# Kernel tuning notes

Hardware: AMD Instinct MI355X
Metric: run time of the kernel (lower is better)

## Reference

```python
import jax, jax.numpy as jnp
import numpy as np

N = 50000
E = 800000
D_IN = 1000
D_H2 = 128  # h_dim * multiple
D_H = 16


def gat_conv(x, src, dst, W, attn_l, attn_r, bias, n):
    """DGL-style GATConv (no dropout, no activation). Returns [n, H, F]."""
    H, F = attn_l.shape
    feat = (x @ W).reshape(n, H, F)                      # [N,H,F]
    el = jnp.sum(feat * attn_l[None], axis=-1)           # [N,H]
    er = jnp.sum(feat * attn_r[None], axis=-1)           # [N,H]
    e = jax.nn.leaky_relu(el[src] + er[dst], 0.2)        # [E,H]
    emax = jax.ops.segment_max(e, dst, num_segments=n)   # [N,H] per-dst softmax max
    ee = jnp.exp(e - emax[dst])                          # [E,H]
    denom = jax.ops.segment_sum(ee, dst, num_segments=n) # [N,H]
    alpha = ee / denom[dst]                              # [E,H]
    msg = feat[src] * alpha[..., None]                   # [E,H,F]
    out = jax.ops.segment_sum(msg, dst, num_segments=n)  # [N,H,F]
    return out + bias.reshape(1, H, F)


def setup_inputs() -> dict:
    key = jax.random.key(0)
    ks = jax.random.split(key, 24)
    rn = lambda k, shp, s=0.05: (jax.random.normal(k, shp, dtype=jnp.float32) * s)
    inp = {
        "x": rn(ks[0], (N, D_IN), 1.0),
        "src": jax.random.randint(ks[1], (E,), 0, N, dtype=jnp.int32),
        "dst": jax.random.randint(ks[2], (E,), 0, N, dtype=jnp.int32),
        "W1": rn(ks[3], (D_IN, D_H2)),
        "al1": rn(ks[4], (1, D_H2)),
        "ar1": rn(ks[5], (1, D_H2)),
        "b1": jnp.zeros((D_H2,), jnp.float32),
        "W2": rn(ks[6], (D_H2, 2 * D_H2)),
        "al2": rn(ks[7], (2, D_H2)),
        "ar2": rn(ks[8], (2, D_H2)),
        "b2": jnp.zeros((2 * D_H2,), jnp.float32),
        "Wm": rn(ks[9], (D_H2, 2 * D_H)),
        "alm": rn(ks[10], (2, D_H)),
        "arm": rn(ks[11], (2, D_H)),
        "bm": jnp.zeros((2 * D_H,), jnp.float32),
        "Wv": rn(ks[12], (D_H2, 2 * D_H)),
        "alv": rn(ks[13], (2, D_H)),
        "arv": rn(ks[14], (2, D_H)),
        "bv": jnp.zeros((2 * D_H,), jnp.float32),
        "eps": rn(ks[15], (N, D_H), 1.0),
    }
    return inp


def reference(x, src, dst, W1, al1, ar1, b1, W2, al2, ar2, b2,
              Wm, alm, arm, bm, Wv, alv, arv, bv, eps):
    n = x.shape[0]
    o = gat_conv(x, src, dst, W1, al1, ar1, b1, n).mean(-2)           # [N,128]
    o = gat_conv(o, src, dst, W2, al2, ar2, b2, n).mean(-2) + o       # residual
    mean = gat_conv(o, src, dst, Wm, alm, arm, bm, n).mean(-2)        # [N,16]
    var = jnp.exp(gat_conv(o, src, dst, Wv, alv, arv, bv, n).mean(-2))
    z = mean + jnp.sqrt(var) * eps                                    # reparameterize
    return z, mean, var
```

## Files before the change

kernel.cpp:

```cpp
#include <hip/hip_runtime.h>
#include <hip/hip_bf16.h>
#include <math.h>

typedef unsigned short u16;
typedef unsigned int u32;
typedef __attribute__((ext_vector_type(8))) __bf16 bf16x8;
typedef __attribute__((ext_vector_type(4))) float f32x4;
typedef __attribute__((ext_vector_type(4))) u32 u32x4;

#define NNODES 50000
#define NEDGES 800000

__device__ __forceinline__ float bf2f(u16 u) {
    union { u32 i; float f; } v; v.i = ((u32)u) << 16; return v.f;
}
__device__ __forceinline__ u16 f2bf(float x) {
    union { float f; u32 i; } v; v.f = x;
    u32 r = v.i + 0x7fffu + ((v.i >> 16) & 1u);
    return (u16)(r >> 16);
}
__device__ __forceinline__ float lrelu(float x) { return x >= 0.f ? x : 0.2f * x; }

__global__ __launch_bounds__(256) void k_zero(int* a, int count) {
    int i = blockIdx.x * 256 + threadIdx.x;
    if (i < count) a[i] = 0;
}

__global__ __launch_bounds__(256) void k_count(const int* __restrict__ dst, int* __restrict__ counts, int e) {
    int i = blockIdx.x * 256 + threadIdx.x;
    if (i < e) atomicAdd(&counts[dst[i]], 1);
}

__global__ __launch_bounds__(256) void k_scan1(const int* __restrict__ counts, int* __restrict__ row_ptr,
                                               int* __restrict__ bsums, int n) {
    __shared__ int tmp[256];
    int t = threadIdx.x, i = blockIdx.x * 256 + t;
    int v = (i < n) ? counts[i] : 0;
    tmp[t] = v; __syncthreads();
    for (int off = 1; off < 256; off <<= 1) {
        int x = 0; if (t >= off) x = tmp[t - off];
        __syncthreads(); tmp[t] += x; __syncthreads();
    }
    if (i < n) row_ptr[i] = tmp[t] - v;
    if (t == 255) bsums[blockIdx.x] = tmp[255];
}

__global__ __launch_bounds__(256) void k_scan2(int* bsums, int nb) {
    __shared__ int tmp[256];
    int t = threadIdx.x;
    int v = (t < nb) ? bsums[t] : 0;
    tmp[t] = v; __syncthreads();
    for (int off = 1; off < 256; off <<= 1) {
        int x = 0; if (t >= off) x = tmp[t - off];
        __syncthreads(); tmp[t] += x; __syncthreads();
    }
    if (t < nb) bsums[t] = tmp[t] - v;
}

__global__ __launch_bounds__(256) void k_scan3(int* __restrict__ row_ptr, const int* __restrict__ bsums,
                                               int n, int total) {
    int i = blockIdx.x * 256 + threadIdx.x;
    if (i < n) row_ptr[i] += bsums[blockIdx.x];
    if (i == 0) row_ptr[n] = total;
}

__global__ __launch_bounds__(256) void k_fill(const int* __restrict__ src, const int* __restrict__ dst,
                                              const int* __restrict__ row_ptr, int* __restrict__ cursor,
                                              int* __restrict__ esrc, int e) {
    int i = blockIdx.x * 256 + threadIdx.x;
    if (i < e) {
        int d = dst[i];
        int p = row_ptr[d] + atomicAdd(&cursor[d], 1);
        esrc[p] = src[i];
    }
}

__global__ __launch_bounds__(256) void k_transpose(const float* __restrict__ W, u16* __restrict__ Wt, int K, int Nn) {
    int i = blockIdx.x * 256 + threadIdx.x;
    if (i < K * Nn) { int k = i / Nn, n = i % Nn; Wt[n * K + k] = f2bf(W[i]); }
}

__device__ __forceinline__ void load_af(const float* __restrict__ arow, int k0, int K, bf16x8& a) {
    if (k0 + 8 <= K) {
        f32x4 a0 = *(const f32x4*)(arow + k0);
        f32x4 a1 = *(const f32x4*)(arow + k0 + 4);
#pragma unroll
        for (int j = 0; j < 4; j++) { a[j] = (__bf16)a0[j]; a[4 + j] = (__bf16)a1[j]; }
    } else {
#pragma unroll
        for (int j = 0; j < 8; j++) a[j] = (__bf16)0.f;
    }
}
__device__ __forceinline__ void load_af(const u16* __restrict__ arow, int k0, int K, bf16x8& a) {
    if (k0 + 8 <= K) a = *(const bf16x8*)(arow + k0);
    else {
#pragma unroll
        for (int j = 0; j < 8; j++) a[j] = (__bf16)0.f;
    }
}

template <typename AT>
__global__ __launch_bounds__(256) void k_gemm_tiled(const AT* __restrict__ A, const u16* __restrict__ Bt,
                                                    u16* __restrict__ C, int M, int Nn, int K) {
    __shared__ __align__(16) u16 lb[2][128 * 40];
    const int tid = threadIdx.x;
    const int wave = tid >> 6, lane = tid & 63;
    const int m = lane & 15, quad = lane >> 4;
    const int row0 = blockIdx.x * 64 + wave * 16;
    const int col0 = blockIdx.y * 128;

    f32x4 acc[8];
#pragma unroll
    for (int t = 0; t < 8; t++)
#pragma unroll
        for (int r = 0; r < 4; r++) acc[t][r] = 0.f;

    int ar = row0 + m; if (ar > M - 1) ar = M - 1;
    const AT* arow = A + (size_t)ar * K;
    const int scol = tid & 127;
    const int sseg = (tid >> 7) * 16;
    const u16* bcol = Bt + (size_t)(col0 + scol) * K;

    const int nsteps = (K + 31) >> 5;

#pragma unroll
    for (int p = 0; p < 2; ++p) {
        int kl = sseg + p * 8;
        u32x4 v = 0;
        if (kl < K) v = *(const u32x4*)(bcol + kl);
        *(u32x4*)&lb[0][scol * 40 + kl] = v;
    }
    bf16x8 acur, anext;
    load_af(arow, quad * 8, K, acur);
    __syncthreads();

    for (int s = 0; s < nsteps; ++s) {
        const int buf = s & 1;
        if (s + 1 < nsteps) {
            const int k0n = (s + 1) * 32;
            load_af(arow, k0n + quad * 8, K, anext);
#pragma unroll
            for (int p = 0; p < 2; ++p) {
                int kl = sseg + p * 8;
                u32x4 v = 0;
                if (k0n + kl < K) v = *(const u32x4*)(bcol + k0n + kl);
                *(u32x4*)&lb[buf ^ 1][scol * 40 + kl] = v;
            }
        }
#pragma unroll
        for (int t = 0; t < 8; ++t) {
            bf16x8 b = *(const bf16x8*)&lb[buf][(t * 16 + m) * 40 + quad * 8];
            acc[t] = __builtin_amdgcn_mfma_f32_16x16x32_bf16(acur, b, acc[t], 0, 0, 0);
        }
        acur = anext;
        __syncthreads();
    }

#pragma unroll
    for (int t = 0; t < 8; t++)
#pragma unroll
        for (int r = 0; r < 4; r++) {
            int row = row0 + quad * 4 + r;
            int col = col0 + t * 16 + m;
            if (row < M) C[(size_t)row * Nn + col] = f2bf(acc[t][r]);
        }
}

template <int NT>
__global__ __launch_bounds__(64) void k_gemm(const u16* __restrict__ A, const u16* __restrict__ Bt,
                                             u16* __restrict__ C, int M, int Nn, int K) {
    int row0 = blockIdx.x * 16;
    int col0 = blockIdx.y * (16 * NT);
    int lane = threadIdx.x;
    int m = lane & 15, quad = lane >> 4;
    f32x4 acc[NT];
#pragma unroll
    for (int t = 0; t < NT; t++)
#pragma unroll
        for (int r = 0; r < 4; r++) acc[t][r] = 0.f;

    const u16* arow = A + (size_t)(row0 + m) * K + quad * 8;
    int full = K >> 5;
    for (int s = 0; s < full; ++s) {
        bf16x8 a = *(const bf16x8*)(arow + s * 32);
#pragma unroll
        for (int t = 0; t < NT; t++) {
            bf16x8 b = *(const bf16x8*)(Bt + (size_t)(col0 + t * 16 + m) * K + s * 32 + quad * 8);
            acc[t] = __builtin_amdgcn_mfma_f32_16x16x32_bf16(a, b, acc[t], 0, 0, 0);
        }
    }
#pragma unroll
    for (int t = 0; t < NT; t++)
#pragma unroll
        for (int r = 0; r < 4; r++) {
            int row = row0 + quad * 4 + r;
            int col = col0 + t * 16 + m;
            if (row < M) C[(size_t)row * Nn + col] = f2bf(acc[t][r]);
        }
}

__global__ __launch_bounds__(256) void k_eler1(const u16* __restrict__ feat, const float* __restrict__ al,
                                               const float* __restrict__ ar, float* __restrict__ el,
                                               float* __restrict__ er, int n) {
    int node = blockIdx.x * 4 + (threadIdx.x >> 6);
    if (node >= n) return;
    int lane = threadIdx.x & 63;
    const u16* fr = feat + (size_t)node * 128;
    float f0 = bf2f(fr[lane]), f1 = bf2f(fr[64 + lane]);
    float pe = f0 * al[lane] + f1 * al[64 + lane];
    float pr = f0 * ar[lane] + f1 * ar[64 + lane];
#pragma unroll
    for (int off = 32; off; off >>= 1) { pe += __shfl_xor(pe, off); pr += __shfl_xor(pr, off); }
    if (lane == 0) { el[node] = pe; er[node] = pr; }
}

__global__ __launch_bounds__(256) void k_eler2(const u16* __restrict__ feat, const float* __restrict__ al,
                                               const float* __restrict__ ar, float* __restrict__ el,
                                               float* __restrict__ er, int n) {
    int node = blockIdx.x * 4 + (threadIdx.x >> 6);
    if (node >= n) return;
    int lane = threadIdx.x & 63;
    const u16* fr = feat + (size_t)node * 256;
#pragma unroll
    for (int h = 0; h < 2; ++h) {
        float f0 = bf2f(fr[h * 128 + lane]), f1 = bf2f(fr[h * 128 + 64 + lane]);
        float pe = f0 * al[h * 128 + lane] + f1 * al[h * 128 + 64 + lane];
        float pr = f0 * ar[h * 128 + lane] + f1 * ar[h * 128 + 64 + lane];
#pragma unroll
        for (int off = 32; off; off >>= 1) { pe += __shfl_xor(pe, off); pr += __shfl_xor(pr, off); }
        if (lane == 0) { el[node * 2 + h] = pe; er[node * 2 + h] = pr; }
    }
}

__global__ __launch_bounds__(256) void k_elermv(const u16* __restrict__ featm, const u16* __restrict__ featv,
                                                const float* __restrict__ alm, const float* __restrict__ arm,
                                                const float* __restrict__ alv, const float* __restrict__ arv,
                                                float* __restrict__ elm, float* __restrict__ erm,
                                                float* __restrict__ elv, float* __restrict__ erv, int n) {
    int node = blockIdx.x * 4 + (threadIdx.x >> 6);
    if (node >= n) return;
    int lane = threadIdx.x & 63;
    int tbl = lane >> 5, j = lane & 31;
    const u16* ft = tbl ? featv : featm;
    const float* al = tbl ? alv : alm;
    const float* ar = tbl ? arv : arm;
    float f = bf2f(ft[(size_t)node * 32 + j]);
    float pe = f * al[j], pr = f * ar[j];
#pragma unroll
    for (int off = 1; off < 16; off <<= 1) { pe += __shfl_xor(pe, off); pr += __shfl_xor(pr, off); }
    if ((lane & 15) == 0) {
        int h = (lane >> 4) & 1;
        float* el = tbl ? elv : elm; float* er = tbl ? erv : erm;
        el[node * 2 + h] = pe; er[node * 2 + h] = pr;
    }
}

__global__ __launch_bounds__(256) void k_agg1(const int* __restrict__ row_ptr, const int* __restrict__ esrc,
                                              const u16* __restrict__ feat, const float* __restrict__ el,
                                              const float* __restrict__ er, const float* __restrict__ bias,
                                              u16* __restrict__ o_bf, int n) {
    int node = blockIdx.x * 4 + (threadIdx.x >> 6);
    if (node >= n) return;
    int lane = threadIdx.x & 63;
    int beg = row_ptr[node], end = row_ptr[node + 1];
    float erd = er[node];
    float mx = -3.0e38f;
    for (int i = beg + lane; i < end; i += 64) mx = fmaxf(mx, el[esrc[i]]);
#pragma unroll
    for (int off = 32; off; off >>= 1) mx = fmaxf(mx, __shfl_xor(mx, off));
    float me = (end > beg) ? lrelu(mx + erd) : 0.f;
    float acc0 = 0.f, acc1 = 0.f, den = 0.f;
    for (int base = beg; base < end; base += 64) {
        int i = base + lane;
        float w = 0.f; int s = 0;
        if (i < end) { s = esrc[i]; w = expf(lrelu(el[s] + erd) - me); }
        den += w;
        int cnt = min(64, end - base);
        int j = 0;
        for (; j + 4 <= cnt; j += 4) {
            float w0 = __shfl(w, j), w1 = __shfl(w, j + 1), w2 = __shfl(w, j + 2), w3 = __shfl(w, j + 3);
            int s0 = __shfl(s, j), s1 = __shfl(s, j + 1), s2 = __shfl(s, j + 2), s3 = __shfl(s, j + 3);
            u32 p0 = ((const u32*)(feat + (size_t)s0 * 128))[lane];
            u32 p1 = ((const u32*)(feat + (size_t)s1 * 128))[lane];
            u32 p2 = ((const u32*)(feat + (size_t)s2 * 128))[lane];
            u32 p3 = ((const u32*)(feat + (size_t)s3 * 128))[lane];
            acc0 += w0 * bf2f((u16)(p0 & 0xffff)) + w1 * bf2f((u16)(p1 & 0xffff))
                  + w2 * bf2f((u16)(p2 & 0xffff)) + w3 * bf2f((u16)(p3 & 0xffff));
            acc1 += w0 * bf2f((u16)(p0 >> 16)) + w1 * bf2f((u16)(p1 >> 16))
                  + w2 * bf2f((u16)(p2 >> 16)) + w3 * bf2f((u16)(p3 >> 16));
        }
        for (; j < cnt; ++j) {
            float wj = __shfl(w, j);
            int sj = __shfl(s, j);
            u32 pv = ((const u32*)(feat + (size_t)sj * 128))[lane];
            acc0 += wj * bf2f((u16)(pv & 0xffff));
            acc1 += wj * bf2f((u16)(pv >> 16));
        }
    }
#pragma unroll
    for (int off = 32; off; off >>= 1) den += __shfl_xor(den, off);
    float inv = (den > 0.f) ? 1.f / den : 0.f;
    float o0 = acc0 * inv + bias[2 * lane];
    float o1 = acc1 * inv + bias[2 * lane + 1];
    u32 pv = (u32)f2bf(o0) | ((u32)f2bf(o1) << 16);
    ((u32*)(o_bf + (size_t)node * 128))[lane] = pv;
}

__global__ __launch_bounds__(256) void k_agg2(const int* __restrict__ row_ptr, const int* __restrict__ esrc,
                                              const u16* __restrict__ feat, const float* __restrict__ el,
                                              const float* __restrict__ er, const float* __restrict__ bias,
                                              const u16* __restrict__ o_in, u16* __restrict__ o2_bf, int n) {
    int node = blockIdx.x * 4 + (threadIdx.x >> 6);
    if (node >= n) return;
    int lane = threadIdx.x & 63;
    int beg = row_ptr[node], end = row_ptr[node + 1];
    float er0 = er[node * 2], er1 = er[node * 2 + 1];
    float mx0 = -3.0e38f, mx1 = -3.0e38f;
    for (int i = beg + lane; i < end; i += 64) {
        int s = esrc[i];
        float2 e2 = *(const float2*)(el + 2 * s);
        mx0 = fmaxf(mx0, e2.x); mx1 = fmaxf(mx1, e2.y);
    }
#pragma unroll
    for (int off = 32; off; off >>= 1) { mx0 = fmaxf(mx0, __shfl_xor(mx0, off)); mx1 = fmaxf(mx1, __shfl_xor(mx1, off)); }
    float me0 = (end > beg) ? lrelu(mx0 + er0) : 0.f;
    float me1 = (end > beg) ? lrelu(mx1 + er1) : 0.f;
    float a00 = 0.f, a01 = 0.f, a10 = 0.f, a11 = 0.f, d0 = 0.f, d1 = 0.f;
    for (int base = beg; base < end; base += 64) {
        int i = base + lane;
        float w0 = 0.f, w1 = 0.f; int s = 0;
        if (i < end) {
            s = esrc[i];
            float2 e2 = *(const float2*)(el + 2 * s);
            w0 = expf(lrelu(e2.x + er0) - me0);
            w1 = expf(lrelu(e2.y + er1) - me1);
        }
        d0 += w0; d1 += w1;
        int cnt = min(64, end - base);
        int j = 0;
        for (; j + 2 <= cnt; j += 2) {
            float w0a = __shfl(w0, j), w1a = __shfl(w1, j), w0b = __shfl(w0, j + 1), w1b = __shfl(w1, j + 1);
            int sa = __shfl(s, j), sb = __shfl(s, j + 1);
            const u32* fa = (const u32*)(feat + (size_t)sa * 256);
            const u32* fb = (const u32*)(feat + (size_t)sb * 256);
            u32 pa0 = fa[lane], pa1 = fa[64 + lane];
            u32 pb0 = fb[lane], pb1 = fb[64 + lane];
            a00 += w0a * bf2f((u16)(pa0 & 0xffff)) + w0b * bf2f((u16)(pb0 & 0xffff));
            a01 += w0a * bf2f((u16)(pa0 >> 16))    + w0b * bf2f((u16)(pb0 >> 16));
            a10 += w1a * bf2f((u16)(pa1 & 0xffff)) + w1b * bf2f((u16)(pb1 & 0xffff));
            a11 += w1a * bf2f((u16)(pa1 >> 16))    + w1b * bf2f((u16)(pb1 >> 16));
        }
        for (; j < cnt; ++j) {
            float w0j = __shfl(w0, j), w1j = __shfl(w1, j);
            int sj = __shfl(s, j);
            const u32* fp = (const u32*)(feat + (size_t)sj * 256);
            u32 p0 = fp[lane], p1 = fp[64 + lane];
            a00 += w0j * bf2f((u16)(p0 & 0xffff)); a01 += w0j * bf2f((u16)(p0 >> 16));
            a10 += w1j * bf2f((u16)(p1 & 0xffff)); a11 += w1j * bf2f((u16)(p1 >> 16));
        }
    }
#pragma unroll
    for (int off = 32; off; off >>= 1) { d0 += __shfl_xor(d0, off); d1 += __shfl_xor(d1, off); }
    float i0 = (d0 > 0.f) ? 1.f / d0 : 0.f, i1 = (d1 > 0.f) ? 1.f / d1 : 0.f;
    int c = 2 * lane;
    float r0 = bf2f(o_in[(size_t)node * 128 + c]), r1 = bf2f(o_in[(size_t)node * 128 + c + 1]);
    float o0 = 0.5f * ((a00 * i0 + bias[c]) + (a10 * i1 + bias[128 + c])) + r0;
    float o1 = 0.5f * ((a01 * i0 + bias[c + 1]) + (a11 * i1 + bias[128 + c + 1])) + r1;
    u32 pv = (u32)f2bf(o0) | ((u32)f2bf(o1) << 16);
    ((u32*)(o2_bf + (size_t)node * 128))[lane] = pv;
}

__global__ __launch_bounds__(256) void k_aggmv(const int* __restrict__ row_ptr, const int* __restrict__ esrc,
                                               const u16* __restrict__ featm, const u16* __restrict__ featv,
                                               const float* __restrict__ elm, const float* __restrict__ erm,
                                               const float* __restrict__ elv, const float* __restrict__ erv,
                                               const float* __restrict__ bm, const float* __restrict__ bv,
                                               const float* __restrict__ eps, float* __restrict__ out, int n) {
    int node = blockIdx.x * 4 + (threadIdx.x >> 6);
    if (node >= n) return;
    int lane = threadIdx.x & 63;
    int f = lane & 15, h = (lane >> 4) & 1, tbl = lane >> 5;
    int beg = row_ptr[node], end = row_ptr[node + 1];
    float erm0 = erm[2 * node], erm1 = erm[2 * node + 1];
    float erv0 = erv[2 * node], erv1 = erv[2 * node + 1];
    float mm0 = -3.0e38f, mm1 = -3.0e38f, mv0 = -3.0e38f, mv1 = -3.0e38f;
    for (int i = beg + lane; i < end; i += 64) {
        int s = esrc[i];
        float2 em = *(const float2*)(elm + 2 * s);
        float2 ev = *(const float2*)(elv + 2 * s);
        mm0 = fmaxf(mm0, em.x); mm1 = fmaxf(mm1, em.y);
        mv0 = fmaxf(mv0, ev.x); mv1 = fmaxf(mv1, ev.y);
    }
#pragma unroll
    for (int off = 32; off; off >>= 1) {
        mm0 = fmaxf(mm0, __shfl_xor(mm0, off)); mm1 = fmaxf(mm1, __shfl_xor(mm1, off));
        mv0 = fmaxf(mv0, __shfl_xor(mv0, off)); mv1 = fmaxf(mv1, __shfl_xor(mv1, off));
    }
    float mem0 = (end > beg) ? lrelu(mm0 + erm0) : 0.f;
    float mem1 = (end > beg) ? lrelu(mm1 + erm1) : 0.f;
    float mev0 = (end > beg) ? lrelu(mv0 + erv0) : 0.f;
    float mev1 = (end > beg) ? lrelu(mv1 + erv1) : 0.f;

    const u16* ftp = tbl ? featv : featm;
    const int fidx = h * 16 + f;
    float accv = 0.f;
    float dm0 = 0.f, dm1 = 0.f, dv0 = 0.f, dv1 = 0.f;
    for (int base = beg; base < end; base += 64) {
        int i = base + lane;
        float wm0 = 0.f, wm1 = 0.f, wv0 = 0.f, wv1 = 0.f; int s = 0;
        if (i < end) {
            s = esrc[i];
            float2 em = *(const float2*)(elm + 2 * s);
            float2 ev = *(const float2*)(elv + 2 * s);
            wm0 = expf(lrelu(em.x + erm0) - mem0);
            wm1 = expf(lrelu(em.y + erm1) - mem1);
            wv0 = expf(lrelu(ev.x + erv0) - mev0);
            wv1 = expf(lrelu(ev.y + erv1) - mev1);
        }
        dm0 += wm0; dm1 += wm1; dv0 += wv0; dv1 += wv1;
        int cnt = min(64, end - base);
        for (int j = 0; j < cnt; ++j) {
            int sj = __shfl(s, j);
            float bm0 = __shfl(wm0, j);
            float bm1 = __shfl(wm1, j);
            float bv0 = __shfl(wv0, j);
            float bv1 = __shfl(wv1, j);
            float wj = tbl ? (h ? bv1 : bv0) : (h ? bm1 : bm0);
            accv += wj * bf2f(ftp[(size_t)sj * 32 + fidx]);
        }
    }
#pragma unroll
    for (int off = 32; off; off >>= 1) {
        dm0 += __shfl_xor(dm0, off); dm1 += __shfl_xor(dm1, off);
        dv0 += __shfl_xor(dv0, off); dv1 += __shfl_xor(dv1, off);
    }
    float den = tbl ? (h ? dv1 : dv0) : (h ? dm1 : dm0);
    float inv = (den > 0.f) ? 1.f / den : 0.f;
    float biasc = tbl ? bv[fidx] : bm[fidx];
    float outc = accv * inv + biasc;
    float hm = 0.5f * (outc + __shfl_xor(outc, 16));
    float meanv = __shfl(hm, f);
    float varp = __shfl(hm, 32 + f);
    if (lane < 16) {
        float var = expf(varp);
        float z = meanv + sqrtf(var) * eps[(size_t)node * 16 + f];
        size_t base = (size_t)node * 16 + f;
        out[base] = z;
        out[(size_t)NNODES * 16 + base] = meanv;
        out[(size_t)2 * NNODES * 16 + base] = var;
    }
}

extern "C" void kernel_launch(void* const* d_in, const int* in_sizes, int n_in,
                              void* d_out, int out_size, void* d_ws, size_t ws_size,
                              hipStream_t stream) {
    const int N = NNODES, E = NEDGES;
    const float* x   = (const float*)d_in[0];
    const int* src   = (const int*)d_in[1];
    const int* dst   = (const int*)d_in[2];
    const float* W1  = (const float*)d_in[3];
    const float* al1 = (const float*)d_in[4];
    const float* ar1 = (const float*)d_in[5];
    const float* b1  = (const float*)d_in[6];
    const float* W2  = (const float*)d_in[7];
    const float* al2 = (const float*)d_in[8];
    const float* ar2 = (const float*)d_in[9];
    const float* b2  = (const float*)d_in[10];
    const float* Wm  = (const float*)d_in[11];
    const float* alm = (const float*)d_in[12];
    const float* arm = (const float*)d_in[13];
    const float* bm  = (const float*)d_in[14];
    const float* Wv  = (const float*)d_in[15];
    const float* alv = (const float*)d_in[16];
    const float* arv = (const float*)d_in[17];
    const float* bv  = (const float*)d_in[18];
    const float* eps = (const float*)d_in[19];
    float* out = (float*)d_out;

    char* ws = (char*)d_ws;
    size_t off = 0;
    auto take = [&](size_t bytes) { size_t r = off; off += (bytes + 255) & ~(size_t)255; return r; };
    int* counts   = (int*)(ws + take((size_t)N * 4));
    int* cursor   = (int*)(ws + take((size_t)N * 4));
    int* row_ptr  = (int*)(ws + take((size_t)(N + 1) * 4));
    int* bsums    = (int*)(ws + take(256 * 4));
    int* esrc     = (int*)(ws + take((size_t)E * 4));
    u16* W1t      = (u16*)(ws + take((size_t)128 * 1000 * 2));
    u16* W2t      = (u16*)(ws + take((size_t)256 * 128 * 2));
    u16* Wmt      = (u16*)(ws + take((size_t)32 * 128 * 2));
    u16* Wvt      = (u16*)(ws + take((size_t)32 * 128 * 2));
    float* el1    = (float*)(ws + take((size_t)N * 4));
    float* er1    = (float*)(ws + take((size_t)N * 4));
    float* el2    = (float*)(ws + take((size_t)N * 2 * 4));
    float* er2    = (float*)(ws + take((size_t)N * 2 * 4));
    float* elm    = (float*)(ws + take((size_t)N * 2 * 4));
    float* erm    = (float*)(ws + take((size_t)N * 2 * 4));
    float* elv    = (float*)(ws + take((size_t)N * 2 * 4));
    float* erv    = (float*)(ws + take((size_t)N * 2 * 4));
    u16* o_bf     = (u16*)(ws + take((size_t)N * 128 * 2));
    u16* o2_bf    = (u16*)(ws + take((size_t)N * 128 * 2));
    u16* R        = (u16*)(ws + take((size_t)N * 256 * 2));
    u16* feat1    = R;
    u16* feat2    = R;
    u16* featm    = R;
    u16* featv    = R + (size_t)N * 32;
    (void)ws_size; (void)n_in; (void)in_sizes; (void)out_size;

    const int nb = (N + 255) / 256;
    const int eb = (E + 255) / 256;
    const int wb = (N + 3) / 4;
    const int gb = (N + 63) / 64;

    k_zero<<<dim3(nb), 256, 0, stream>>>(counts, N);
    k_zero<<<dim3(nb), 256, 0, stream>>>(cursor, N);
    k_count<<<dim3(eb), 256, 0, stream>>>(dst, counts, E);
    k_scan1<<<dim3(nb), 256, 0, stream>>>(counts, row_ptr, bsums, N);
    k_scan2<<<dim3(1), 256, 0, stream>>>(bsums, nb);
    k_scan3<<<dim3(nb), 256, 0, stream>>>(row_ptr, bsums, N, E);
    k_fill<<<dim3(eb), 256, 0, stream>>>(src, dst, row_ptr, cursor, esrc, E);

    k_transpose<<<dim3((1000 * 128 + 255) / 256), 256, 0, stream>>>(W1, W1t, 1000, 128);
    k_transpose<<<dim3((128 * 256 + 255) / 256), 256, 0, stream>>>(W2, W2t, 128, 256);
    k_transpose<<<dim3((128 * 32 + 255) / 256), 256, 0, stream>>>(Wm, Wmt, 128, 32);
    k_transpose<<<dim3((128 * 32 + 255) / 256), 256, 0, stream>>>(Wv, Wvt, 128, 32);

    k_gemm_tiled<float><<<dim3(gb, 1), 256, 0, stream>>>(x, W1t, feat1, N, 128, 1000);
    k_eler1<<<dim3(wb), 256, 0, stream>>>(feat1, al1, ar1, el1, er1, N);
    k_agg1<<<dim3(wb), 256, 0, stream>>>(row_ptr, esrc, feat1, el1, er1, b1, o_bf, N);

    k_gemm_tiled<u16><<<dim3(gb, 2), 256, 0, stream>>>(o_bf, W2t, feat2, N, 256, 128);
    k_eler2<<<dim3(wb), 256, 0, stream>>>(feat2, al2, ar2, el2, er2, N);
    k_agg2<<<dim3(wb), 256, 0, stream>>>(row_ptr, esrc, feat2, el2, er2, b2, o_bf, o2_bf, N);

    k_gemm<2><<<dim3(N / 16, 1), 64, 0, stream>>>(o2_bf, Wmt, featm, N, 32, 128);
    k_gemm<2><<<dim3(N / 16, 1), 64, 0, stream>>>(o2_bf, Wvt, featv, N, 32, 128);
    k_elermv<<<dim3(wb), 256, 0, stream>>>(featm, featv, alm, arm, alv, arv, elm, erm, elv, erv, N);
    k_aggmv<<<dim3(wb), 256, 0, stream>>>(row_ptr, esrc, featm, featv, elm, erm, elv, erv,
                                          bm, bv, eps, out, N);
}
```

Baseline: 682.9 us.

## Reorder layer-2 GAT to aggregate before projecting by W2

Layer 2 now folds the attention vectors into W2 (ul = W2·al, ur = W2·ar), so el/er come straight from the 128-wide input rather than the 256-wide projected features. Aggregation gathers the 128-wide o rows per head, and a single GEMM with a concatenated, head-averaged W2 (K=256, N=128) applies the projection, bias and residual in its epilogue. This halves the bytes gathered per edge in the aggregation, which is the costly random-access phase. In exchange it writes a 256-wide intermediate and adds small precompute kernels, and rounding order changes because the bf16 aggregate is projected afterwards.

```diff
diff --git a/kernel.cpp b/kernel.cpp
--- a/kernel.cpp
+++ b/kernel.cpp
@@ -80,6 +80,35 @@
     if (i < K * Nn) { int k = i / Nn, n = i % Nn; Wt[n * K + k] = f2bf(W[i]); }
 }
 
+__global__ __launch_bounds__(256) void k_attnvec(const float* __restrict__ W2, const float* __restrict__ al2,
+                                                 const float* __restrict__ ar2, const float* __restrict__ b2,
+                                                 float* __restrict__ ul, float* __restrict__ ur,
+                                                 float* __restrict__ bmean) {
+    int t = threadIdx.x;
+    int h = t >> 7, k = t & 127;
+    const float* wrow = W2 + (size_t)k * 256 + h * 128;
+    const float* alh = al2 + h * 128;
+    const float* arh = ar2 + h * 128;
+    float sl = 0.f, sr = 0.f;
+    for (int f = 0; f < 128; f += 4) {
+        f32x4 w = *(const f32x4*)(wrow + f);
+        f32x4 a = *(const f32x4*)(alh + f);
+        f32x4 r = *(const f32x4*)(arh + f);
+#pragma unroll
+        for (int q = 0; q < 4; q++) { sl += w[q] * a[q]; sr += w[q] * r[q]; }
+    }
+    ul[t] = sl; ur[t] = sr;
+    if (t < 128) bmean[t] = 0.5f * (b2[t] + b2[128 + t]);
+}
+
+__global__ __launch_bounds__(256) void k_makeWc(const float* __restrict__ W2, u16* __restrict__ Wct) {
+    int i = blockIdx.x * 256 + threadIdx.x;
+    if (i < 128 * 256) {
+        int f = i >> 8, c = i & 255, h = c >> 7, k = c & 127;
+        Wct[i] = f2bf(0.5f * W2[(size_t)k * 256 + h * 128 + f]);
+    }
+}
+
 __device__ __forceinline__ void load_af(const float* __restrict__ arow, int k0, int K, bf16x8& a) {
     if (k0 + 8 <= K) {
         f32x4 a0 = *(const f32x4*)(arow + k0);
@@ -99,9 +128,11 @@
     }
 }
 
-template <typename AT>
+template <typename AT, bool EPI>
 __global__ __launch_bounds__(256) void k_gemm_tiled(const AT* __restrict__ A, const u16* __restrict__ Bt,
-                                                    u16* __restrict__ C, int M, int Nn, int K) {
+                                                    u16* __restrict__ C, int M, int Nn, int K,
+                                                    const float* __restrict__ bias,
+                                                    const u16* __restrict__ resid) {
     __shared__ __align__(16) u16 lb[2][128 * 40];
     const int tid = threadIdx.x;
     const int wave = tid >> 6, lane = tid & 63;
@@ -162,7 +193,11 @@
         for (int r = 0; r < 4; r++) {
             int row = row0 + quad * 4 + r;
             int col = col0 + t * 16 + m;
-            if (row < M) C[(size_t)row * Nn + col] = f2bf(acc[t][r]);
+            if (row < M) {
+                float v = acc[t][r];
+                if (EPI) v += bias[col] + bf2f(resid[(size_t)row * Nn + col]);
+                C[(size_t)row * Nn + col] = f2bf(v);
+            }
         }
 }
 
@@ -214,18 +249,18 @@
     if (lane == 0) { el[node] = pe; er[node] = pr; }
 }
 
-__global__ __launch_bounds__(256) void k_eler2(const u16* __restrict__ feat, const float* __restrict__ al,
-                                               const float* __restrict__ ar, float* __restrict__ el,
-                                               float* __restrict__ er, int n) {
+__global__ __launch_bounds__(256) void k_eler2o(const u16* __restrict__ o_in, const float* __restrict__ ul,
+                                                const float* __restrict__ ur, float* __restrict__ el,
+                                                float* __restrict__ er, int n) {
     int node = blockIdx.x * 4 + (threadIdx.x >> 6);
     if (node >= n) return;
     int lane = threadIdx.x & 63;
-    const u16* fr = feat + (size_t)node * 256;
+    const u16* fr = o_in + (size_t)node * 128;
+    float f0 = bf2f(fr[lane]), f1 = bf2f(fr[64 + lane]);
 #pragma unroll
     for (int h = 0; h < 2; ++h) {
-        float f0 = bf2f(fr[h * 128 + lane]), f1 = bf2f(fr[h * 128 + 64 + lane]);
-        float pe = f0 * al[h * 128 + lane] + f1 * al[h * 128 + 64 + lane];
-        float pr = f0 * ar[h * 128 + lane] + f1 * ar[h * 128 + 64 + lane];
+        float pe = f0 * ul[h * 128 + lane] + f1 * ul[h * 128 + 64 + lane];
+        float pr = f0 * ur[h * 128 + lane] + f1 * ur[h * 128 + 64 + lane];
 #pragma unroll
         for (int off = 32; off; off >>= 1) { pe += __shfl_xor(pe, off); pr += __shfl_xor(pr, off); }
         if (lane == 0) { el[node * 2 + h] = pe; er[node * 2 + h] = pr; }
@@ -306,10 +341,9 @@
     ((u32*)(o_bf + (size_t)node * 128))[lane] = pv;
 }
 
-__global__ __launch_bounds__(256) void k_agg2(const int* __restrict__ row_ptr, const int* __restrict__ esrc,
-                                              const u16* __restrict__ feat, const float* __restrict__ el,
-                                              const float* __restrict__ er, const float* __restrict__ bias,
-                                              const u16* __restrict__ o_in, u16* __restrict__ o2_bf, int n) {
+__global__ __launch_bounds__(256) void k_agg2o(const int* __restrict__ row_ptr, const int* __restrict__ esrc,
+                                               const u16* __restrict__ o_in, const float* __restrict__ el,
+                                               const float* __restrict__ er, u16* __restrict__ agg, int n) {
     int node = blockIdx.x * 4 + (threadIdx.x >> 6);
     if (node >= n) return;
     int lane = threadIdx.x & 63;
@@ -338,36 +372,40 @@
         d0 += w0; d1 += w1;
         int cnt = min(64, end - base);
         int j = 0;
-        for (; j + 2 <= cnt; j += 2) {
-            float w0a = __shfl(w0, j), w1a = __shfl(w1, j), w0b = __shfl(w0, j + 1), w1b = __shfl(w1, j + 1);
-            int sa = __shfl(s, j), sb = __shfl(s, j + 1);
-            const u32* fa = (const u32*)(feat + (size_t)sa * 256);
-            const u32* fb = (const u32*)(feat + (size_t)sb * 256);
-            u32 pa0 = fa[lane], pa1 = fa[64 + lane];
-            u32 pb0 = fb[lane], pb1 = fb[64 + lane];
-            a00 += w0a * bf2f((u16)(pa0 & 0xffff)) + w0b * bf2f((u16)(pb0 & 0xffff));
-            a01 += w0a * bf2f((u16)(pa0 >> 16))    + w0b * bf2f((u16)(pb0 >> 16));
-            a10 += w1a * bf2f((u16)(pa1 & 0xffff)) + w1b * bf2f((u16)(pb1 & 0xffff));
-            a11 += w1a * bf2f((u16)(pa1 >> 16))    + w1b * bf2f((u16)(pb1 >> 16));
+        for (; j + 4 <= cnt; j += 4) {
+            float w0a = __shfl(w0, j), w0b = __shfl(w0, j + 1), w0c = __shfl(w0, j + 2), w0d = __shfl(w0, j + 3);
+            float w1a = __shfl(w1, j), w1b = __shfl(w1, j + 1), w1c = __shfl(w1, j + 2), w1d = __shfl(w1, j + 3);
+            int sa = __shfl(s, j), sb = __shfl(s, j + 1), sc = __shfl(s, j + 2), sd = __shfl(s, j + 3);
+            u32 pa = ((const u32*)(o_in + (size_t)sa * 128))[lane];
+            u32 pb = ((const u32*)(o_in + (size_t)sb * 128))[lane];
+            u32 pc = ((const u32*)(o_in + (size_t)sc * 128))[lane];
+            u32 pd = ((const u32*)(o_in + (size_t)sd * 128))[lane];
+            float la = bf2f((u16)(pa & 0xffff)), ha = bf2f((u16)(pa >> 16));
+            float lb = bf2f((u16)(pb & 0xffff)), hb = bf2f((u16)(pb >> 16));
+            float lc = bf2f((u16)(pc & 0xffff)), hc = bf2f((u16)(pc >> 16));
+            float ld = bf2f((u16)(pd & 0xffff)), hd = bf2f((u16)(pd >> 16));
+            a00 += w0a * la + w0b * lb + w0c * lc + w0d * ld;
+            a01 += w0a * ha + w0b * hb + w0c * hc + w0d * hd;
+            a10 += w1a * la + w1b * lb + w1c * lc + w1d * ld;
+            a11 += w1a * ha + w1b * hb + w1c * hc + w1d * hd;
         }
         for (; j < cnt; ++j) {
             float w0j = __shfl(w0, j), w1j = __shfl(w1, j);
             int sj = __shfl(s, j);
-            const u32* fp = (const u32*)(feat + (size_t)sj * 256);
-            u32 p0 = fp[lane], p1 = fp[64 + lane];
-            a00 += w0j * bf2f((u16)(p0 & 0xffff)); a01 += w0j * bf2f((u16)(p0 >> 16));
-            a10 += w1j * bf2f((u16)(p1 & 0xffff)); a11 += w1j * bf2f((u16)(p1 >> 16));
+            u32 pv = ((const u32*)(o_in + (size_t)sj * 128))[lane];
+            float lo = bf2f((u16)(pv & 0xffff)), hi = bf2f((u16)(pv >> 16));
+            a00 += w0j * lo; a01 += w0j * hi;
+            a10 += w1j * lo; a11 += w1j * hi;
         }
     }
 #pragma unroll
     for (int off = 32; off; off >>= 1) { d0 += __shfl_xor(d0, off); d1 += __shfl_xor(d1, off); }
     float i0 = (d0 > 0.f) ? 1.f / d0 : 0.f, i1 = (d1 > 0.f) ? 1.f / d1 : 0.f;
-    int c = 2 * lane;
-    float r0 = bf2f(o_in[(size_t)node * 128 + c]), r1 = bf2f(o_in[(size_t)node * 128 + c + 1]);
-    float o0 = 0.5f * ((a00 * i0 + bias[c]) + (a10 * i1 + bias[128 + c])) + r0;
-    float o1 = 0.5f * ((a01 * i0 + bias[c + 1]) + (a11 * i1 + bias[128 + c + 1])) + r1;
-    u32 pv = (u32)f2bf(o0) | ((u32)f2bf(o1) << 16);
-    ((u32*)(o2_bf + (size_t)node * 128))[lane] = pv;
+    u32 p0 = (u32)f2bf(a00 * i0) | ((u32)f2bf(a01 * i0) << 16);
+    u32 p1 = (u32)f2bf(a10 * i1) | ((u32)f2bf(a11 * i1) << 16);
+    u32* aw = (u32*)(agg + (size_t)node * 256);
+    aw[lane] = p0;
+    aw[64 + lane] = p1;
 }
 
 __global__ __launch_bounds__(256) void k_aggmv(const int* __restrict__ row_ptr, const int* __restrict__ esrc,
@@ -486,9 +524,12 @@
     int* bsums    = (int*)(ws + take(256 * 4));
     int* esrc     = (int*)(ws + take((size_t)E * 4));
     u16* W1t      = (u16*)(ws + take((size_t)128 * 1000 * 2));
-    u16* W2t      = (u16*)(ws + take((size_t)256 * 128 * 2));
+    u16* Wct      = (u16*)(ws + take((size_t)128 * 256 * 2));
     u16* Wmt      = (u16*)(ws + take((size_t)32 * 128 * 2));
     u16* Wvt      = (u16*)(ws + take((size_t)32 * 128 * 2));
+    float* ul2    = (float*)(ws + take(256 * 4));
+    float* ur2    = (float*)(ws + take(256 * 4));
+    float* bmean  = (float*)(ws + take(128 * 4));
     float* el1    = (float*)(ws + take((size_t)N * 4));
     float* er1    = (float*)(ws + take((size_t)N * 4));
     float* el2    = (float*)(ws + take((size_t)N * 2 * 4));
@@ -501,7 +542,7 @@
     u16* o2_bf    = (u16*)(ws + take((size_t)N * 128 * 2));
     u16* R        = (u16*)(ws + take((size_t)N * 256 * 2));
     u16* feat1    = R;
-    u16* feat2    = R;
+    u16* agg      = R;
     u16* featm    = R;
     u16* featv    = R + (size_t)N * 32;
     (void)ws_size; (void)n_in; (void)in_sizes; (void)out_size;
@@ -520,17 +561,18 @@
     k_fill<<<dim3(eb), 256, 0, stream>>>(src, dst, row_ptr, cursor, esrc, E);
 
     k_transpose<<<dim3((1000 * 128 + 255) / 256), 256, 0, stream>>>(W1, W1t, 1000, 128);
-    k_transpose<<<dim3((128 * 256 + 255) / 256), 256, 0, stream>>>(W2, W2t, 128, 256);
+    k_makeWc<<<dim3(128), 256, 0, stream>>>(W2, Wct);
+    k_attnvec<<<dim3(1), 256, 0, stream>>>(W2, al2, ar2, b2, ul2, ur2, bmean);
     k_transpose<<<dim3((128 * 32 + 255) / 256), 256, 0, stream>>>(Wm, Wmt, 128, 32);
     k_transpose<<<dim3((128 * 32 + 255) / 256), 256, 0, stream>>>(Wv, Wvt, 128, 32);
 
-    k_gemm_tiled<float><<<dim3(gb, 1), 256, 0, stream>>>(x, W1t, feat1, N, 128, 1000);
+    k_gemm_tiled<float, false><<<dim3(gb, 1), 256, 0, stream>>>(x, W1t, feat1, N, 128, 1000, nullptr, nullptr);
     k_eler1<<<dim3(wb), 256, 0, stream>>>(feat1, al1, ar1, el1, er1, N);
     k_agg1<<<dim3(wb), 256, 0, stream>>>(row_ptr, esrc, feat1, el1, er1, b1, o_bf, N);
 
-    k_gemm_tiled<u16><<<dim3(gb, 2), 256, 0, stream>>>(o_bf, W2t, feat2, N, 256, 128);
-    k_eler2<<<dim3(wb), 256, 0, stream>>>(feat2, al2, ar2, el2, er2, N);
-    k_agg2<<<dim3(wb), 256, 0, stream>>>(row_ptr, esrc, feat2, el2, er2, b2, o_bf, o2_bf, N);
+    k_eler2o<<<dim3(wb), 256, 0, stream>>>(o_bf, ul2, ur2, el2, er2, N);
+    k_agg2o<<<dim3(wb), 256, 0, stream>>>(row_ptr, esrc, o_bf, el2, er2, agg, N);
+    k_gemm_tiled<u16, true><<<dim3(gb, 1), 256, 0, stream>>>(agg, Wct, o2_bf, N, 128, 256, bmean, o_bf);
 
     k_gemm<2><<<dim3(N / 16, 1), 64, 0, stream>>>(o2_bf, Wmt, featm, N, 32, 128);
     k_gemm<2><<<dim3(N / 16, 1), 64, 0, stream>>>(o2_bf, Wvt, featv, N, 32, 128);
```

New measurement: 678.2 us. Within noise of the previous version (-0.7%).
